# Kernel tuning notes

Hardware: AMD Instinct MI355X
Metric: run time of the kernel (lower is better)

The kernel has to match this reference:

```python
import jax, jax.numpy as jnp
import numpy as np

HEADS = 16
EPS = 1e-5

def _ln(t):
    # LayerNorm over last axis, no affine params
    mu = jnp.mean(t, axis=-1, keepdims=True)
    var = jnp.var(t, axis=-1, keepdims=True)
    return (t - mu) / jnp.sqrt(var + EPS)

def setup_inputs() -> dict:
    key = jax.random.key(0)
    ks = jax.random.split(key, 8)
    b, n, dim, mlp_dim = 4, 2048, 1024, 4096
    s = lambda d: 1.0 / np.sqrt(d)
    return {
        "x": jax.random.normal(ks[0], (b, n, dim), dtype=jnp.float32),
        "Wqkv": jax.random.uniform(ks[1], (dim, 3 * dim), jnp.float32, -s(dim), s(dim)),
        "W1": jax.random.uniform(ks[2], (dim, mlp_dim), jnp.float32, -s(dim), s(dim)),
        "b1": jax.random.uniform(ks[3], (mlp_dim,), jnp.float32, -s(dim), s(dim)),
        "W2": jax.random.uniform(ks[4], (mlp_dim, dim), jnp.float32, -s(mlp_dim), s(mlp_dim)),
        "b2": jax.random.uniform(ks[5], (dim,), jnp.float32, -s(mlp_dim), s(mlp_dim)),
        "Wout": jax.random.uniform(ks[6], (dim, dim), jnp.float32, -s(dim), s(dim)),
        "bout": jax.random.uniform(ks[7], (dim,), jnp.float32, -s(dim), s(dim)),
    }

def reference(x, Wqkv, W1, b1, W2, b2, Wout, bout):
    b, n, dim = x.shape
    h = HEADS
    d = dim // h
    scale = dim ** (-0.5)  # NOTE: module scales by full dim, not head_dim
    qkv = x @ Wqkv  # [b, n, 3*dim]
    qkv = qkv.reshape(b, n, 3, h, d).transpose(2, 0, 3, 1, 4)  # [3, b, h, n, d]
    q, k, v = qkv[0], qkv[1], qkv[2]
    q, k = _ln(q), _ln(k)
    dots = jnp.einsum('bhid,bhjd->bhij', q, k) * scale
    attn = jax.nn.softmax(dots, axis=-1)
    attn_v = jnp.einsum('bhij,bhjd->bhid', attn, v)
    attn_v = attn_v.transpose(0, 2, 1, 3).reshape(b, n, dim)
    attn_out = attn_v @ Wout + bout
    parallel = jax.nn.gelu(x @ W1 + b1, approximate=False) @ W2 + b2
    return _ln(attn_out + parallel)
```

## Files before the change

kernel.cpp:

```cpp
#include <hip/hip_runtime.h>

typedef __attribute__((ext_vector_type(8))) short s16x8;
typedef __attribute__((ext_vector_type(4))) short s16x4;
typedef __attribute__((ext_vector_type(4))) float f32x4;
typedef __attribute__((ext_vector_type(16))) float f32x16;
typedef __attribute__((ext_vector_type(2))) unsigned uint2v;

#define DEVINL __device__ __forceinline__

DEVINL float b2f(short u){ return __uint_as_float(((unsigned)(unsigned short)u) << 16); }
DEVINL short f2bf(float f){
  unsigned u = __float_as_uint(f);
  u += 0x7fffu + ((u >> 16) & 1u);
  return (short)(u >> 16);
}
DEVINL unsigned cvtpk(float lo, float hi){
  unsigned r;
  asm("v_cvt_pk_bf16_f32 %0, %1, %2" : "=v"(r) : "v"(lo), "v"(hi));
  return r;
}
DEVINL float max3f(float a, float b, float c){
  float r; asm("v_max3_f32 %0, %1, %2, %3" : "=v"(r) : "v"(a), "v"(b), "v"(c)); return r;
}

#if __has_builtin(__builtin_amdgcn_exp2f)
#define EXP2F __builtin_amdgcn_exp2f
#else
#define EXP2F exp2f
#endif

DEVINL f32x4 mfma32(s16x8 a, s16x8 b, f32x4 c){
  return __builtin_amdgcn_mfma_f32_16x16x32_bf16(a, b, c, 0, 0, 0);
}
DEVINL f32x16 mfma3216(s16x8 a, s16x8 b, f32x16 c){
  return __builtin_amdgcn_mfma_f32_32x32x16_bf16(a, b, c, 0, 0, 0);
}

DEVINL uint2v pl32swap(unsigned a, unsigned b){
#if __has_builtin(__builtin_amdgcn_permlane32_swap)
  return __builtin_amdgcn_permlane32_swap(a, b, false, false);
#else
  asm volatile("v_permlane32_swap_b32 %0, %1" : "+v"(a), "+v"(b));
  uint2v r; r[0] = a; r[1] = b; return r;
#endif
}

typedef const unsigned __attribute__((address_space(1)))* gas1;
typedef unsigned __attribute__((address_space(3)))* las3;
DEVINL void gload16(const short* g, short* l){
  __builtin_amdgcn_global_load_lds((gas1)g, (las3)l, 16, 0, 0);
}

#define CFENCE asm volatile("" ::: "memory")
#define PBAR  do{ CFENCE; __builtin_amdgcn_sched_barrier(0); __builtin_amdgcn_s_barrier(); \
                  __builtin_amdgcn_sched_barrier(0); CFENCE; }while(0)
#define RBAR  __builtin_amdgcn_s_barrier()
#define LGKM0 do{ asm volatile("s_waitcnt lgkmcnt(0)" ::: "memory"); \
                  __builtin_amdgcn_sched_barrier(0); }while(0)
#define VMW8 asm volatile("s_waitcnt vmcnt(8)" ::: "memory")
#define VMW4 asm volatile("s_waitcnt vmcnt(4)" ::: "memory")
#define VMW0 asm volatile("s_waitcnt vmcnt(0)" ::: "memory")
#define PRIO1 __builtin_amdgcn_s_setprio(1)
#define PRIO0 __builtin_amdgcn_s_setprio(0)

static const int Bc   = 4;
static const int Nc   = 2048;
static const int DIM  = 1024;
static const int Tc   = Bc * Nc;
static const int MLP  = 4096;
static const int D3   = 3072;

static const size_t OFF_XB    = 0;
static const size_t OFF_WQKVT = OFF_XB    + 16777216;
static const size_t OFF_W1T   = OFF_WQKVT + 6291456;
static const size_t OFF_W2T   = OFF_W1T   + 8388608;
static const size_t OFF_WOUTT = OFF_W2T   + 8388608;
static const size_t OFF_QKV   = OFF_WOUTT + 2097152;
static const size_t OFF_QLN   = OFF_QKV   + 50331648;
static const size_t OFF_KLN   = OFF_QLN   + 16777216;
static const size_t OFF_VT    = OFF_KLN   + 16777216;
static const size_t OFF_ATTNV = OFF_VT    + 16777216;
static const size_t OFF_H     = OFF_QKV;
static const size_t OFF_S2    = OFF_KLN;

__global__ __launch_bounds__(256) void conv_x(const float* __restrict__ x, short* __restrict__ xb){
  size_t i = ((size_t)blockIdx.x * 256 + threadIdx.x) * 8;
  f32x4 v0 = *(const f32x4*)(x + i);
  f32x4 v1 = *(const f32x4*)(x + i + 4);
  s16x8 o;
#pragma unroll
  for (int j = 0; j < 4; ++j){ o[j] = f2bf(v0[j]); o[4+j] = f2bf(v1[j]); }
  *(s16x8*)(xb + i) = o;
}

__global__ __launch_bounds__(256) void transpose_conv(const float* __restrict__ W, short* __restrict__ Wt,
                                                      int K, int N){
  __shared__ float tile[32][33];
  int ntx = N >> 5;
  int tx = blockIdx.x % ntx, ty = blockIdx.x / ntx;
  int r = threadIdx.x >> 3, c = (threadIdx.x & 7) * 4;
  f32x4 v = *(const f32x4*)(W + (size_t)(ty*32 + r)*N + tx*32 + c);
  tile[r][c] = v[0]; tile[r][c+1] = v[1]; tile[r][c+2] = v[2]; tile[r][c+3] = v[3];
  __syncthreads();
  s16x4 o;
#pragma unroll
  for (int j = 0; j < 4; ++j) o[j] = f2bf(tile[c+j][r]);
  *(s16x4*)(Wt + (size_t)(tx*32 + r)*K + ty*32 + c) = o;
}

template<int ACT>
__global__ __launch_bounds__(512, 2) void gemm8q(const short* __restrict__ A, const short* __restrict__ Bt,
                                                 short* __restrict__ C, const float* __restrict__ bias,
                                                 int M, int N, int K){
  __shared__ short lds[65536];
  short* Ab = lds;
  short* Bb = lds + 32768;

  const int tid = threadIdx.x;
  const int w = tid >> 6, lane = tid & 63;
  const int lr = lane & 15, g = lane >> 4;
  const int wr = w >> 2, wc = w & 3;
  const int NT = K >> 6;

  const int nbn = N >> 8;
  const int cpx = gridDim.x >> 3;
  const int bid = (int)blockIdx.x;
  const int sw = (bid & 7)*cpx + (bid >> 3);
  const int bm = sw / nbn, bn = sw % nbn;

  const int l2 = lane >> 2;
  const int gsw = ((lane & 3) - ((lane >> 3) & 3)) & 3;
  const int cof = gsw * 8;
  const int qsw8 = ((g + (lr >> 1)) & 3) * 8;

  const short* ap0 = A  + (size_t)(bm*256 + w*16 + l2)*K + cof;
  const short* bp0 = Bt + (size_t)(bn*256 + w*16 + l2)*K + cof;

#define STA2(buf, T_, kk) do{ \
    gload16(ap0 + (size_t)(T_)*64 + (kk)*32,                   Ab + (((buf)*2+(kk))*2+0)*4096 + w*512); \
    gload16(ap0 + (size_t)128*K + (size_t)(T_)*64 + (kk)*32,   Ab + (((buf)*2+(kk))*2+1)*4096 + w*512); }while(0)
#define STB2(buf, T_, kk) do{ \
    gload16(bp0 + (size_t)(T_)*64 + (kk)*32,                   Bb + ((buf)*2+(kk))*8192 + w*512); \
    gload16(bp0 + (size_t)128*K + (size_t)(T_)*64 + (kk)*32,   Bb + ((buf)*2+(kk))*8192 + 4096 + w*512); }while(0)
#define LA(buf, kk, mi) (*(const s16x8*)&Ab[(((buf)*2+(kk))*2+wr)*4096 + ((mi)*16 + lr)*32 + qsw8])
#define LB(buf, kk, ni) (*(const s16x8*)&Bb[((buf)*2+(kk))*8192 + (wc*64 + (ni)*16 + lr)*32 + qsw8])

  f32x4 acc[8][4] = {};

  STA2(0,0,0); STB2(0,0,0);
  STA2(0,0,1); STB2(0,0,1);
  VMW0;
  RBAR;

  for (int t = 0; t < NT; ++t){
    const int buf = t & 1, nb = buf ^ 1;
    const bool more = (t + 1 < NT);

    {
      s16x8 af[8];
#pragma unroll
      for (int mi = 0; mi < 8; ++mi) af[mi] = LA(buf, 0, mi);
      s16x8 b0 = LB(buf, 0, 0), b1 = LB(buf, 0, 1);
      if (more) STA2(nb, t+1, 0);
      RBAR;
      LGKM0;
      PRIO1;
#pragma unroll
      for (int mi = 0; mi < 8; ++mi){
        acc[mi][0] = mfma32(af[mi], b0, acc[mi][0]);
        acc[mi][1] = mfma32(af[mi], b1, acc[mi][1]);
      }
      PRIO0;
      RBAR;
    }
    {
      s16x8 af[8];
#pragma unroll
      for (int mi = 0; mi < 8; ++mi) af[mi] = LA(buf, 0, mi);
      s16x8 b0 = LB(buf, 0, 2), b1 = LB(buf, 0, 3);
      if (more) STB2(nb, t+1, 0);
      RBAR;
      LGKM0;
      PRIO1;
#pragma unroll
      for (int mi = 0; mi < 8; ++mi){
        acc[mi][2] = mfma32(af[mi], b0, acc[mi][2]);
        acc[mi][3] = mfma32(af[mi], b1, acc[mi][3]);
      }
      PRIO0;
      if (more){ VMW4; } else { VMW0; }
      RBAR;
    }
    {
      s16x8 af[8];
#pragma unroll
      for (int mi = 0; mi < 8; ++mi) af[mi] = LA(buf, 1, mi);
      s16x8 b0 = LB(buf, 1, 0), b1 = LB(buf, 1, 1);
      if (more) STA2(nb, t+1, 1);
      RBAR;
      LGKM0;
      PRIO1;
#pragma unroll
      for (int mi = 0; mi < 8; ++mi){
        acc[mi][0] = mfma32(af[mi], b0, acc[mi][0]);
        acc[mi][1] = mfma32(af[mi], b1, acc[mi][1]);
      }
      PRIO0;
      RBAR;
    }
    {
      s16x8 af[8];
#pragma unroll
      for (int mi = 0; mi < 8; ++mi) af[mi] = LA(buf, 1, mi);
      s16x8 b0 = LB(buf, 1, 2), b1 = LB(buf, 1, 3);
      if (more) STB2(nb, t+1, 1);
      RBAR;
      LGKM0;
      PRIO1;
#pragma unroll
      for (int mi = 0; mi < 8; ++mi){
        acc[mi][2] = mfma32(af[mi], b0, acc[mi][2]);
        acc[mi][3] = mfma32(af[mi], b1, acc[mi][3]);
      }
      PRIO0;
      if (more){ VMW4; }
      RBAR;
    }
  }
#undef STA2
#undef STB2
#undef LA
#undef LB

#pragma unroll
  for (int mi = 0; mi < 8; ++mi){
#pragma unroll
    for (int ni = 0; ni < 4; ++ni){
      const int col = wc*64 + ni*16 + lr;
      const float bv = bias ? bias[bn*256 + col] : 0.f;
      f32x4 v = acc[mi][ni];
#pragma unroll
      for (int ii = 0; ii < 4; ++ii){
        float val = v[ii] + bv;
        if constexpr (ACT) val = 0.5f*val*(1.f + erff(val*0.70710678118f));
        lds[(wr*128 + mi*16 + 4*g + ii)*256 + col] = f2bf(val);
      }
    }
  }
  __syncthreads();
  const size_t crow0 = (size_t)bm * 256;
  const int ch = (tid & 31) * 8;
#pragma unroll
  for (int p = 0; p < 16; ++p){
    const int row = p*16 + (tid >> 5);
    *(s16x8*)&C[(crow0 + row)*N + bn*256 + ch] = *(const s16x8*)&lds[row*256 + ch];
  }
}

template<int ACT, int FUSED>
__global__ __launch_bounds__(256, 2) void gemmCF(const short* __restrict__ A, const short* __restrict__ A2,
                                                 const short* __restrict__ Bt, const short* __restrict__ Bt2,
                                                 short* __restrict__ C,
                                                 const float* __restrict__ bias, const float* __restrict__ bias2,
                                                 int M, int N, int K1, int K2){
  __shared__ short lds[32768];

  const int tid = threadIdx.x;
  const int w = tid >> 6, lane = tid & 63;
  const int lr = lane & 15, g = lane >> 4;
  const int wr = w >> 1, wc = w & 1;
  const int NT1 = K1 >> 6;
  const int NT = NT1 + (FUSED ? (K2 >> 6) : 0);
  const int NIT = NT >> 1;

  const int nbn = N >> 7;
  const int cpx = gridDim.x >> 3;
  const int bid = (int)blockIdx.x;
  const int sw = (bid & 7)*cpx + (bid >> 3);
  const int nbn8 = nbn >> 3;
  const int T8 = sw >> 6, t64 = sw & 63;
  const int bm = (T8 / nbn8)*8 + (t64 >> 3);
  const int bn = (T8 % nbn8)*8 + (t64 & 7);

  const int l2 = lane >> 2;
  const int gsw = ((lane & 3) - ((lane >> 3) & 3)) & 3;
  const int cof = gsw * 8;
  const int qsw8 = ((g + (lr >> 1)) & 3) * 8;

  const short* ap0h = A  + (size_t)(bm*128 + w*16 + l2)*K1 + cof;
  const short* bp0h = Bt + (size_t)(bn*128 + w*16 + l2)*K1 + cof;
  const short* ap0a = FUSED ? (A2  + (size_t)(bm*128 + w*16 + l2)*K2 + cof) : nullptr;
  const short* bp0a = FUSED ? (Bt2 + (size_t)(bn*128 + w*16 + l2)*K2 + cof) : nullptr;

  auto stA = [&](int s, int T_, int kk){
    short* d0 = lds + s*4096 + w*512;
    if (FUSED && T_ >= NT1){
      size_t off = (size_t)(T_ - NT1)*64 + kk*32;
      gload16(ap0a + off, d0);
      gload16(ap0a + (size_t)64*K2 + off, d0 + 2048);
    } else {
      size_t off = (size_t)T_*64 + kk*32;
      gload16(ap0h + off, d0);
      gload16(ap0h + (size_t)64*K1 + off, d0 + 2048);
    }
  };
  auto stB = [&](int s, int T_, int kk){
    short* d0 = lds + 16384 + s*4096 + w*512;
    if (FUSED && T_ >= NT1){
      size_t off = (size_t)(T_ - NT1)*64 + kk*32;
      gload16(bp0a + off, d0);
      gload16(bp0a + (size_t)64*K2 + off, d0 + 2048);
    } else {
      size_t off = (size_t)T_*64 + kk*32;
      gload16(bp0h + off, d0);
      gload16(bp0h + (size_t)64*K1 + off, d0 + 2048);
    }
  };

#define LDA(s, mi) (*(const s16x8*)&lds[(s)*4096 + (wr*64 + (mi)*16 + lr)*32 + qsw8])
#define LDB(s, ni) (*(const s16x8*)&lds[16384 + (s)*4096 + (wc*64 + (ni)*16 + lr)*32 + qsw8])

  f32x4 acc[4][4] = {};
#define MM(ai, r) \
  acc[r][0]=mfma32(ai,b0,acc[r][0]); acc[r][1]=mfma32(ai,b1,acc[r][1]); \
  acc[r][2]=mfma32(ai,b2,acc[r][2]); acc[r][3]=mfma32(ai,b3,acc[r][3]);
#define RD(s) s16x8 a0=LDA(s,0),a1=LDA(s,1),a2=LDA(s,2),a3=LDA(s,3), \
                    b0=LDB(s,0),b1=LDB(s,1),b2=LDB(s,2),b3=LDB(s,3);
#define MM16 MM(a0,0) MM(a1,1) MM(a2,2) MM(a3,3)

  stA(0,0,0); stB(0,0,0);
  stA(1,0,1); stB(1,0,1);
  stA(2,1,0); stB(2,1,0);
  VMW8;
  PBAR;

  for (int i = 0; i < NIT; ++i){
    const int t = i << 1;
    const bool more = (i + 1 < NIT);
    {
      RD(0)
      stA(3, t+1, 1); stB(3, t+1, 1);
      PBAR; PRIO1; MM16 PRIO0;
      VMW8;
      PBAR;
    }
    {
      RD(1)
      if (more){ stA(0, t+2, 0); stB(0, t+2, 0); }
      PBAR; PRIO1; MM16 PRIO0;
      if (more){ VMW8; } else { VMW4; }
      PBAR;
    }
    {
      RD(2)
      if (more){ stA(1, t+2, 1); stB(1, t+2, 1); }
      PBAR; PRIO1; MM16 PRIO0;
      if (more){ VMW8; } else { VMW0; }
      PBAR;
    }
    {
      RD(3)
      if (more){ stA(2, t+3, 0); stB(2, t+3, 0); }
      PBAR; PRIO1; MM16 PRIO0;
      if (more){ VMW8; }
      PBAR;
    }
  }
#undef MM
#undef RD
#undef MM16
#undef LDA
#undef LDB

#pragma unroll
  for (int a = 0; a < 4; ++a){
#pragma unroll
    for (int ni = 0; ni < 4; ++ni){
      const int col = wc*64 + ni*16 + lr;
      float bv = bias ? bias[bn*128 + col] : 0.f;
      if (FUSED && bias2) bv += bias2[bn*128 + col];
      f32x4 v = acc[a][ni];
#pragma unroll
      for (int ii = 0; ii < 4; ++ii){
        float val = v[ii] + bv;
        if constexpr (ACT) val = 0.5f*val*(1.f + erff(val*0.70710678118f));
        lds[(wr*64 + a*16 + 4*g + ii)*128 + col] = f2bf(val);
      }
    }
  }
  __syncthreads();
  const size_t crow0 = (size_t)bm * 128;
  const int ch = (tid & 15) * 8;
#pragma unroll
  for (int p = 0; p < 8; ++p){
    const int row = p*16 + (tid >> 4);
    *(s16x8*)&C[(crow0 + row)*N + bn*128 + ch] = *(const s16x8*)&lds[row*128 + ch];
  }
}

__global__ __launch_bounds__(256) void ln_reorg(const short* __restrict__ qkv, short* __restrict__ qln,
                                                short* __restrict__ kln, short* __restrict__ vtb){
  __shared__ short vtile[64*72];
  int bh = blockIdx.x >> 5, tch = blockIdx.x & 31;
  int b = bh >> 4, h = bh & 15;
  int tq = threadIdx.x >> 2, j = threadIdx.x & 3;
  size_t row = (size_t)b*Nc + tch*64 + tq;
  const short* base = qkv + row*D3 + h*64 + j*16;
  size_t orow = ((size_t)bh*Nc + tch*64 + tq)*64 + j*16;

#pragma unroll
  for (int part = 0; part < 2; ++part){
    const short* src = base + part*DIM;
    s16x8 u0 = *(const s16x8*)src;
    s16x8 u1 = *(const s16x8*)(src + 8);
    float f[16]; float s = 0.f, sq = 0.f;
#pragma unroll
    for (int i = 0; i < 8; ++i){ f[i] = b2f(u0[i]); f[8+i] = b2f(u1[i]); }
#pragma unroll
    for (int i = 0; i < 16; ++i){ s += f[i]; sq += f[i]*f[i]; }
    s  += __shfl_xor(s, 1);  s  += __shfl_xor(s, 2);
    sq += __shfl_xor(sq, 1); sq += __shfl_xor(sq, 2);
    float mu = s * (1.f/64.f);
    float var = sq * (1.f/64.f) - mu*mu;
    float inv = rsqrtf(var + 1e-5f) * (part == 0 ? 0.04508422003f : 1.f);
    s16x8 o0, o1;
#pragma unroll
    for (int i = 0; i < 8; ++i){ o0[i] = f2bf((f[i]-mu)*inv); o1[i] = f2bf((f[8+i]-mu)*inv); }
    short* dst = (part == 0 ? qln : kln) + orow;
    *(s16x8*)dst = o0; *(s16x8*)(dst + 8) = o1;
  }

  s16x8 v0 = *(const s16x8*)(base + 2*DIM);
  s16x8 v1 = *(const s16x8*)(base + 2*DIM + 8);
  *(s16x8*)&vtile[tq*72 + j*16]     = v0;
  *(s16x8*)&vtile[tq*72 + j*16 + 8] = v1;
  __syncthreads();
  s16x8 o0, o1;
#pragma unroll
  for (int i = 0; i < 8; ++i){
    o0[i] = vtile[(j*16 + i)*72 + tq];
    o1[i] = vtile[(j*16 + 8 + i)*72 + tq];
  }
  short* vdst = vtb + ((size_t)bh*64 + tq)*Nc + tch*64 + j*16;
  *(s16x8*)vdst = o0; *(s16x8*)(vdst + 8) = o1;
}

__global__ __launch_bounds__(256) void attn_kern(const short* __restrict__ qln, const short* __restrict__ kln,
                                                 const short* __restrict__ vtb, short* __restrict__ attnv){
  __shared__ short Ks[2][64*72];
  __shared__ short Vs[2][64*72];
  const int tid = threadIdx.x;
  const int bh = blockIdx.x >> 4, qt = blockIdx.x & 15;
  const int b = bh >> 4, h = bh & 15;
  const int w = tid >> 6, lane = tid & 63;
  const int lq = lane & 31, hi = lane >> 5;
  const int qrow = qt*128 + w*32 + lq;

  const short* qp = qln + ((size_t)bh*Nc + qrow)*64 + hi*8;
  s16x8 qf[4];
#pragma unroll
  for (int m = 0; m < 4; ++m) qf[m] = *(const s16x8*)(qp + m*16);

  f32x16 o0 = {0,0,0,0,0,0,0,0,0,0,0,0,0,0,0,0};
  f32x16 o1 = {0,0,0,0,0,0,0,0,0,0,0,0,0,0,0,0};
  float mrun = -INFINITY, l = 0.f;

  const int sr = tid >> 3;
  const int sc = (tid & 7) * 8;
  const short* kb0 = kln + (size_t)bh*Nc*64;
  const short* vb0 = vtb + (size_t)bh*64*Nc;

  s16x8 kr0, kr1, vr0, vr1;
  {
    kr0 = *(const s16x8*)(kb0 + (size_t)sr*64 + sc);
    kr1 = *(const s16x8*)(kb0 + (size_t)(32 + sr)*64 + sc);
    vr0 = *(const s16x8*)(vb0 + (size_t)sr*Nc + sc);
    vr1 = *(const s16x8*)(vb0 + (size_t)(32 + sr)*Nc + sc);
  }

  for (int kt = 0; kt < 32; ++kt){
    const int cur = kt & 1;
    *(s16x8*)&Ks[cur][sr*72 + sc]        = kr0;
    *(s16x8*)&Ks[cur][(32 + sr)*72 + sc] = kr1;
    *(s16x8*)&Vs[cur][sr*72 + sc]        = vr0;
    *(s16x8*)&Vs[cur][(32 + sr)*72 + sc] = vr1;
    __syncthreads();
    if (kt + 1 < 32){
      const short* kb = kb0 + (size_t)(kt+1)*64*64;
      const short* vb = vb0 + (kt+1)*64;
      kr0 = *(const s16x8*)(kb + (size_t)sr*64 + sc);
      kr1 = *(const s16x8*)(kb + (size_t)(32 + sr)*64 + sc);
      vr0 = *(const s16x8*)(vb + (size_t)sr*Nc + sc);
      vr1 = *(const s16x8*)(vb + (size_t)(32 + sr)*Nc + sc);
    }

    f32x16 st0 = {0,0,0,0,0,0,0,0,0,0,0,0,0,0,0,0};
    f32x16 st1 = {0,0,0,0,0,0,0,0,0,0,0,0,0,0,0,0};
#pragma unroll
    for (int m = 0; m < 4; ++m){
      s16x8 kf0 = *(const s16x8*)&Ks[cur][ lq      *72 + m*16 + hi*8];
      s16x8 kf1 = *(const s16x8*)&Ks[cur][(32 + lq)*72 + m*16 + hi*8];
      st0 = mfma3216(kf0, qf[m], st0);
      st1 = mfma3216(kf1, qf[m], st1);
    }

    float cmax = max3f(st0[0], st0[1], st0[2]);
    cmax = max3f(cmax, st0[3], st0[4]);   cmax = max3f(cmax, st0[5], st0[6]);
    cmax = max3f(cmax, st0[7], st0[8]);   cmax = max3f(cmax, st0[9], st0[10]);
    cmax = max3f(cmax, st0[11], st0[12]); cmax = max3f(cmax, st0[13], st0[14]);
    cmax = max3f(cmax, st0[15], st1[0]);  cmax = max3f(cmax, st1[1], st1[2]);
    cmax = max3f(cmax, st1[3], st1[4]);   cmax = max3f(cmax, st1[5], st1[6]);
    cmax = max3f(cmax, st1[7], st1[8]);   cmax = max3f(cmax, st1[9], st1[10]);
    cmax = max3f(cmax, st1[11], st1[12]); cmax = max3f(cmax, st1[13], st1[14]);
    cmax = fmaxf(cmax, st1[15]);
    cmax = fmaxf(cmax, __shfl_xor(cmax, 32));
    if (__any(cmax > mrun + 8.f)){
      float mnew = fmaxf(mrun, cmax);
      float fr = EXP2F(mrun - mnew);
      l *= fr;
#pragma unroll
      for (int r = 0; r < 16; ++r){ o0[r] *= fr; o1[r] *= fr; }
      mrun = mnew;
    }
    float p0[16], p1[16];
#pragma unroll
    for (int r = 0; r < 16; ++r){
      p0[r] = EXP2F(st0[r] - mrun); l += p0[r];
      p1[r] = EXP2F(st1[r] - mrun); l += p1[r];
    }

#pragma unroll
    for (int kc = 0; kc < 2; ++kc){
      const float* p = kc ? p1 : p0;
#pragma unroll
      for (int kh = 0; kh < 2; ++kh){
        int r0 = kh*8;
        unsigned wa = cvtpk(p[r0+0], p[r0+1]);
        unsigned wb = cvtpk(p[r0+4], p[r0+5]);
        unsigned wc2 = cvtpk(p[r0+2], p[r0+3]);
        unsigned wd = cvtpk(p[r0+6], p[r0+7]);
        uint2v s1 = pl32swap(wa, wb);
        uint2v s2 = pl32swap(wc2, wd);
        union { unsigned u[4]; s16x8 v; } pu;
        pu.u[0] = s1[0]; pu.u[1] = s2[0]; pu.u[2] = s1[1]; pu.u[3] = s2[1];
        s16x8 vf0 = *(const s16x8*)&Vs[cur][ lq      *72 + kc*32 + kh*16 + hi*8];
        s16x8 vf1 = *(const s16x8*)&Vs[cur][(32 + lq)*72 + kc*32 + kh*16 + hi*8];
        o0 = mfma3216(vf0, pu.v, o0);
        o1 = mfma3216(vf1, pu.v, o1);
      }
    }
  }

  l += __shfl_xor(l, 32);
  float inv = 1.f / l;
  short* orow = attnv + ((size_t)(b*Nc + qrow))*DIM + h*64;
#pragma unroll
  for (int r = 0; r < 16; r += 2){
    int dv = (r&3) + 8*(r>>2) + 4*hi;
    *(unsigned*)&orow[dv]      = cvtpk(o0[r]*inv, o0[r+1]*inv);
    *(unsigned*)&orow[32 + dv] = cvtpk(o1[r]*inv, o1[r+1]*inv);
  }
}

__global__ __launch_bounds__(256) void final_ln(const short* __restrict__ s2, float* __restrict__ out){
  __shared__ float red[16];
  int row = blockIdx.x, tid = threadIdx.x;
  size_t base = (size_t)row*DIM + tid*4;
  s16x4 a = *(const s16x4*)(s2 + base);
  float v[4]; float s = 0.f, sq = 0.f;
#pragma unroll
  for (int i = 0; i < 4; ++i){ v[i] = b2f(a[i]); s += v[i]; sq += v[i]*v[i]; }
#pragma unroll
  for (int m = 1; m < 64; m <<= 1){ s += __shfl_xor(s, m); sq += __shfl_xor(sq, m); }
  int wv = tid >> 6;
  if ((tid & 63) == 0){ red[wv] = s; red[8 + wv] = sq; }
  __syncthreads();
  if (tid == 0){
    float S = red[0] + red[1] + red[2] + red[3];
    float Q = red[8] + red[9] + red[10] + red[11];
    float mu = S * (1.f/1024.f);
    float var = Q * (1.f/1024.f) - mu*mu;
    red[12] = mu; red[13] = rsqrtf(var + 1e-5f);
  }
  __syncthreads();
  float mu = red[12], inv = red[13];
#pragma unroll
  for (int i = 0; i < 4; ++i) out[base + i] = (v[i] - mu) * inv;
}

extern "C" void kernel_launch(void* const* d_in, const int* in_sizes, int n_in,
                              void* d_out, int out_size, void* d_ws, size_t ws_size,
                              hipStream_t stream){
  const float* x    = (const float*)d_in[0];
  const float* Wqkv = (const float*)d_in[1];
  const float* W1   = (const float*)d_in[2];
  const float* b1   = (const float*)d_in[3];
  const float* W2   = (const float*)d_in[4];
  const float* b2   = (const float*)d_in[5];
  const float* Wout = (const float*)d_in[6];
  const float* bout = (const float*)d_in[7];
  float* out = (float*)d_out;
  char* ws = (char*)d_ws;

  short* xb    = (short*)(ws + OFF_XB);
  short* wqkvt = (short*)(ws + OFF_WQKVT);
  short* w1t   = (short*)(ws + OFF_W1T);
  short* w2t   = (short*)(ws + OFF_W2T);
  short* woutt = (short*)(ws + OFF_WOUTT);
  short* qkv   = (short*)(ws + OFF_QKV);
  short* qln   = (short*)(ws + OFF_QLN);
  short* kln   = (short*)(ws + OFF_KLN);
  short* vtb   = (short*)(ws + OFF_VT);
  short* attnv = (short*)(ws + OFF_ATTNV);
  short* hbuf  = (short*)(ws + OFF_H);
  short* s2    = (short*)(ws + OFF_S2);

  conv_x<<<4096, 256, 0, stream>>>(x, xb);
  transpose_conv<<<(DIM/32)*(D3/32),  256, 0, stream>>>(Wqkv, wqkvt, DIM, D3);
  transpose_conv<<<(DIM/32)*(MLP/32), 256, 0, stream>>>(W1, w1t, DIM, MLP);
  transpose_conv<<<(MLP/32)*(DIM/32), 256, 0, stream>>>(W2, w2t, MLP, DIM);
  transpose_conv<<<(DIM/32)*(DIM/32), 256, 0, stream>>>(Wout, woutt, DIM, DIM);

  gemm8q<0><<<(Tc/256)*(D3/256), 512, 0, stream>>>(xb, wqkvt, qkv, nullptr, Tc, D3, DIM);
  ln_reorg<<<64*32, 256, 0, stream>>>(qkv, qln, kln, vtb);
  attn_kern<<<64*16, 256, 0, stream>>>(qln, kln, vtb, attnv);

  gemm8q<1><<<(Tc/256)*(MLP/256), 512, 0, stream>>>(xb, w1t, hbuf, b1, Tc, MLP, DIM);
  gemmCF<0,1><<<(Tc/128)*(DIM/128), 256, 0, stream>>>(hbuf, attnv, w2t, woutt, s2,
                                                      b2, bout, Tc, DIM, MLP, DIM);

  final_ln<<<Tc, 256, 0, stream>>>(s2, out);
}
```

Before: 439.0 us.

## Merge GEMM sub-phases into two per k-tile and relax launch bounds

The 256x256 bf16 GEMM used for the QKV and W1 projections now runs two phases per 64-wide k-tile instead of four. Each phase loads all four B fragments and issues the A and B prefetch together, which halves the barriers and LDS A-fragment reloads per tile. Global pointers are advanced incrementally instead of recomputed from the tile index. Launch bounds drop from 2 to 1 blocks per CU, giving the compiler more registers for the extra B fragments, at the risk of lower occupancy and less latency hiding. The prologue now waits with VMW4 instead of VMW0, which may be a hazard if the first tile's data is not fully resident before the barrier.

New measurement: 426.1 us. 1.03x faster.

```diff
diff --git a/kernel.cpp b/kernel.cpp
--- a/kernel.cpp
+++ b/kernel.cpp
@@ -109,7 +109,7 @@
 }
 
 template<int ACT>
-__global__ __launch_bounds__(512, 2) void gemm8q(const short* __restrict__ A, const short* __restrict__ Bt,
+__global__ __launch_bounds__(512, 1) void gemmRX(const short* __restrict__ A, const short* __restrict__ Bt,
                                                  short* __restrict__ C, const float* __restrict__ bias,
                                                  int M, int N, int K){
   __shared__ short lds[65536];
@@ -128,28 +128,30 @@
   const int sw = (bid & 7)*cpx + (bid >> 3);
   const int bm = sw / nbn, bn = sw % nbn;
 
-  const int l2 = lane >> 2;
+  const int l4 = lane >> 2;
   const int gsw = ((lane & 3) - ((lane >> 3) & 3)) & 3;
   const int cof = gsw * 8;
   const int qsw8 = ((g + (lr >> 1)) & 3) * 8;
 
-  const short* ap0 = A  + (size_t)(bm*256 + w*16 + l2)*K + cof;
-  const short* bp0 = Bt + (size_t)(bn*256 + w*16 + l2)*K + cof;
-
-#define STA2(buf, T_, kk) do{ \
-    gload16(ap0 + (size_t)(T_)*64 + (kk)*32,                   Ab + (((buf)*2+(kk))*2+0)*4096 + w*512); \
-    gload16(ap0 + (size_t)128*K + (size_t)(T_)*64 + (kk)*32,   Ab + (((buf)*2+(kk))*2+1)*4096 + w*512); }while(0)
-#define STB2(buf, T_, kk) do{ \
-    gload16(bp0 + (size_t)(T_)*64 + (kk)*32,                   Bb + ((buf)*2+(kk))*8192 + w*512); \
-    gload16(bp0 + (size_t)128*K + (size_t)(T_)*64 + (kk)*32,   Bb + ((buf)*2+(kk))*8192 + 4096 + w*512); }while(0)
-#define LA(buf, kk, mi) (*(const s16x8*)&Ab[(((buf)*2+(kk))*2+wr)*4096 + ((mi)*16 + lr)*32 + qsw8])
-#define LB(buf, kk, ni) (*(const s16x8*)&Bb[((buf)*2+(kk))*8192 + (wc*64 + (ni)*16 + lr)*32 + qsw8])
+  const size_t aK128 = (size_t)128 * K;
+  const short* agA = A  + (size_t)(bm*256 + w*16 + l4)*K + cof;
+  const short* agB = Bt + (size_t)(bn*256 + w*16 + l4)*K + cof;
+
+#define STA_RX(nb, kk) do{ \
+    gload16(agA + (kk)*32,         Ab + ((nb)*2+(kk))*8192 + w*512); \
+    gload16(agA + aK128 + (kk)*32, Ab + ((nb)*2+(kk))*8192 + 4096 + w*512); }while(0)
+#define STB_RX(nb, kk) do{ \
+    gload16(agB + (kk)*32,         Bb + ((nb)*2+(kk))*8192 + w*512); \
+    gload16(agB + aK128 + (kk)*32, Bb + ((nb)*2+(kk))*8192 + 4096 + w*512); }while(0)
+#define LA_RX(buf, kk, mi) (*(const s16x8*)&Ab[((buf)*2+(kk))*8192 + (wr*128 + (mi)*16 + lr)*32 + qsw8])
+#define LB_RX(buf, kk, ni) (*(const s16x8*)&Bb[((buf)*2+(kk))*8192 + (wc*64 + (ni)*16 + lr)*32 + qsw8])
 
   f32x4 acc[8][4] = {};
 
-  STA2(0,0,0); STB2(0,0,0);
-  STA2(0,0,1); STB2(0,0,1);
-  VMW0;
+  STA_RX(0,0); STB_RX(0,0);
+  STA_RX(0,1); STB_RX(0,1);
+  agA += 64; agB += 64;
+  VMW4;
   RBAR;
 
   for (int t = 0; t < NT; ++t){
@@ -159,9 +161,9 @@
     {
       s16x8 af[8];
 #pragma unroll
-      for (int mi = 0; mi < 8; ++mi) af[mi] = LA(buf, 0, mi);
-      s16x8 b0 = LB(buf, 0, 0), b1 = LB(buf, 0, 1);
-      if (more) STA2(nb, t+1, 0);
+      for (int mi = 0; mi < 8; ++mi) af[mi] = LA_RX(buf, 0, mi);
+      s16x8 b0 = LB_RX(buf,0,0), b1 = LB_RX(buf,0,1), b2 = LB_RX(buf,0,2), b3 = LB_RX(buf,0,3);
+      if (more){ STA_RX(nb,0); STB_RX(nb,0); }
       RBAR;
       LGKM0;
       PRIO1;
@@ -169,23 +171,8 @@
       for (int mi = 0; mi < 8; ++mi){
         acc[mi][0] = mfma32(af[mi], b0, acc[mi][0]);
         acc[mi][1] = mfma32(af[mi], b1, acc[mi][1]);
-      }
-      PRIO0;
-      RBAR;
-    }
-    {
-      s16x8 af[8];
-#pragma unroll
-      for (int mi = 0; mi < 8; ++mi) af[mi] = LA(buf, 0, mi);
-      s16x8 b0 = LB(buf, 0, 2), b1 = LB(buf, 0, 3);
-      if (more) STB2(nb, t+1, 0);
-      RBAR;
-      LGKM0;
-      PRIO1;
-#pragma unroll
-      for (int mi = 0; mi < 8; ++mi){
-        acc[mi][2] = mfma32(af[mi], b0, acc[mi][2]);
-        acc[mi][3] = mfma32(af[mi], b1, acc[mi][3]);
+        acc[mi][2] = mfma32(af[mi], b2, acc[mi][2]);
+        acc[mi][3] = mfma32(af[mi], b3, acc[mi][3]);
       }
       PRIO0;
       if (more){ VMW4; } else { VMW0; }
@@ -194,9 +181,9 @@
     {
       s16x8 af[8];
 #pragma unroll
-      for (int mi = 0; mi < 8; ++mi) af[mi] = LA(buf, 1, mi);
-      s16x8 b0 = LB(buf, 1, 0), b1 = LB(buf, 1, 1);
-      if (more) STA2(nb, t+1, 1);
+      for (int mi = 0; mi < 8; ++mi) af[mi] = LA_RX(buf, 1, mi);
+      s16x8 b0 = LB_RX(buf,1,0), b1 = LB_RX(buf,1,1), b2 = LB_RX(buf,1,2), b3 = LB_RX(buf,1,3);
+      if (more){ STA_RX(nb,1); STB_RX(nb,1); }
       RBAR;
       LGKM0;
       PRIO1;
@@ -204,33 +191,19 @@
       for (int mi = 0; mi < 8; ++mi){
         acc[mi][0] = mfma32(af[mi], b0, acc[mi][0]);
         acc[mi][1] = mfma32(af[mi], b1, acc[mi][1]);
-      }
-      PRIO0;
-      RBAR;
-    }
-    {
-      s16x8 af[8];
-#pragma unroll
-      for (int mi = 0; mi < 8; ++mi) af[mi] = LA(buf, 1, mi);
-      s16x8 b0 = LB(buf, 1, 2), b1 = LB(buf, 1, 3);
-      if (more) STB2(nb, t+1, 1);
-      RBAR;
-      LGKM0;
-      PRIO1;
-#pragma unroll
-      for (int mi = 0; mi < 8; ++mi){
-        acc[mi][2] = mfma32(af[mi], b0, acc[mi][2]);
-        acc[mi][3] = mfma32(af[mi], b1, acc[mi][3]);
+        acc[mi][2] = mfma32(af[mi], b2, acc[mi][2]);
+        acc[mi][3] = mfma32(af[mi], b3, acc[mi][3]);
       }
       PRIO0;
       if (more){ VMW4; }
       RBAR;
-    }
-  }
-#undef STA2
-#undef STB2
-#undef LA
-#undef LB
+      agA += 64; agB += 64;
+    }
+  }
+#undef STA_RX
+#undef STB_RX
+#undef LA_RX
+#undef LB_RX
 
 #pragma unroll
   for (int mi = 0; mi < 8; ++mi){
@@ -621,11 +594,11 @@
   transpose_conv<<<(MLP/32)*(DIM/32), 256, 0, stream>>>(W2, w2t, MLP, DIM);
   transpose_conv<<<(DIM/32)*(DIM/32), 256, 0, stream>>>(Wout, woutt, DIM, DIM);
 
-  gemm8q<0><<<(Tc/256)*(D3/256), 512, 0, stream>>>(xb, wqkvt, qkv, nullptr, Tc, D3, DIM);
+  gemmRX<0><<<(Tc/256)*(D3/256), 512, 0, stream>>>(xb, wqkvt, qkv, nullptr, Tc, D3, DIM);
   ln_reorg<<<64*32, 256, 0, stream>>>(qkv, qln, kln, vtb);
   attn_kern<<<64*16, 256, 0, stream>>>(qln, kln, vtb, attnv);
 
-  gemm8q<1><<<(Tc/256)*(MLP/256), 512, 0, stream>>>(xb, w1t, hbuf, b1, Tc, MLP, DIM);
+  gemmRX<1><<<(Tc/256)*(MLP/256), 512, 0, stream>>>(xb, w1t, hbuf, b1, Tc, MLP, DIM);
   gemmCF<0,1><<<(Tc/128)*(DIM/128), 256, 0, stream>>>(hbuf, attnv, w2t, woutt, s2,
                                                       b2, bout, Tc, DIM, MLP, DIM);
 
```
